# Optimization experiments

Hardware: AMD Instinct MI355X
Metric: run time of the kernel (lower is better)

The kernel has to match this reference:

```python
import jax, jax.numpy as jnp
import numpy as np

N_HEAD = 12
N_EMBD = 768

def setup_inputs() -> dict:
    key = jax.random.key(0)
    ks = jax.random.split(key, 5)
    B, T, C = 4, 2048, N_EMBD
    x = jax.random.normal(ks[0], (B, T, C), dtype=jnp.float32)
    # PyTorch Linear default init ~ U(-1/sqrt(fan_in), 1/sqrt(fan_in)); use small normals for a clean baseline
    s = 1.0 / np.sqrt(C)
    W_attn = jax.random.uniform(ks[1], (C, 3 * C), minval=-s, maxval=s, dtype=jnp.float32)
    b_attn = jax.random.uniform(ks[2], (3 * C,), minval=-s, maxval=s, dtype=jnp.float32)
    W_o = jax.random.uniform(ks[3], (C, C), minval=-s, maxval=s, dtype=jnp.float32)
    b_o = jax.random.uniform(ks[4], (C,), minval=-s, maxval=s, dtype=jnp.float32)
    return {"x": x, "W_attn": W_attn, "b_attn": b_attn, "W_o": W_o, "b_o": b_o}

def reference(x, W_attn, b_attn, W_o, b_o):
    B, T, C = x.shape
    H = N_HEAD
    D = C // H  # head dim
    qkv = x @ W_attn + b_attn                      # [B,T,3C]
    q, k, v = jnp.split(qkv, 3, axis=-1)           # each [B,T,C]
    q = q.reshape(B, T, H, D).transpose(0, 2, 1, 3)  # [B,H,T,D]
    k = k.reshape(B, T, H, D).transpose(0, 2, 1, 3)
    v = v.reshape(B, T, H, D).transpose(0, 2, 1, 3)
    att = jnp.einsum('bhqd,bhkd->bhqk', q, k) / jnp.sqrt(jnp.asarray(D, x.dtype))
    causal = jnp.tril(jnp.ones((T, T), dtype=bool))
    att = jnp.where(causal, att, jnp.asarray(-jnp.inf, att.dtype))
    att = jax.nn.softmax(att, axis=-1)             # dropout=0.0 -> identity
    y = jnp.einsum('bhqk,bhkd->bhqd', att, v)      # [B,H,T,D]
    y = y.transpose(0, 2, 1, 3).reshape(B, T, C)   # [B,T,C]
    return y @ W_o + b_o
```

## Files before the change

### kernel.cpp

```cpp
#include <hip/hip_runtime.h>
#include <hip/hip_bf16.h>

#define NHEAD 12
#define TSEQ 2048
#define CEMB 768
#define DHEAD 64
#define NBATCH 4

typedef __attribute__((ext_vector_type(8))) short bf16x8;
typedef __attribute__((ext_vector_type(4))) float f32x4;

__device__ __forceinline__ ushort f2bf(float f) {
  union { float f; unsigned u; } v; v.f = f;
  unsigned u = v.u;
  u += 0x7FFFu + ((u >> 16) & 1u);
  return (ushort)(u >> 16);
}

__device__ __forceinline__ unsigned cvt_pk_bf16(float lo, float hi) {
  unsigned r;
  asm("v_cvt_pk_bf16_f32 %0, %1, %2" : "=v"(r) : "v"(lo), "v"(hi));
  return r;
}

__device__ __forceinline__ float exp2_raw(float x) {
  float r;
  asm("v_exp_f32 %0, %1" : "=v"(r) : "v"(x));
  return r;
}

__device__ __forceinline__ void lds_fence() {
  asm volatile("s_waitcnt lgkmcnt(0)" ::: "memory");
  __builtin_amdgcn_sched_barrier(0);
}

__global__ __launch_bounds__(256)
void prep(const float* __restrict__ x, ushort* __restrict__ xb,
          const float* __restrict__ Wa, ushort* __restrict__ WaT,
          const float* __restrict__ Wo, ushort* __restrict__ WoT)
{
  __shared__ float tile[32][33];
  const int bid = blockIdx.x, t = threadIdx.x;
  if (bid < 3072) {
    int i = (bid * 256 + t) * 8;
    float4 v0 = *(const float4*)(x + i);
    float4 v1 = *(const float4*)(x + i + 4);
    bf16x8 wv;
    wv[0] = (short)f2bf(v0.x); wv[1] = (short)f2bf(v0.y);
    wv[2] = (short)f2bf(v0.z); wv[3] = (short)f2bf(v0.w);
    wv[4] = (short)f2bf(v1.x); wv[5] = (short)f2bf(v1.y);
    wv[6] = (short)f2bf(v1.z); wv[7] = (short)f2bf(v1.w);
    *(bf16x8*)(xb + i) = wv;
    return;
  }
  const int b2 = bid - 3072;
  const int bx = b2 % 96, by = b2 / 96;
  const int tx = t & 31, ty = t >> 5;
  const float* src; ushort* dst; int C, c0;
  if (bx < 72) { src = Wa; dst = WaT; C = 3 * CEMB; c0 = bx * 32; }
  else         { src = Wo; dst = WoT; C = CEMB;     c0 = (bx - 72) * 32; }
  const int r0 = by * 32;
#pragma unroll
  for (int j = 0; j < 4; ++j)
    tile[ty + j * 8][tx] = src[(size_t)(r0 + ty + j * 8) * C + c0 + tx];
  __syncthreads();
#pragma unroll
  for (int j = 0; j < 4; ++j)
    dst[(size_t)(c0 + ty + j * 8) * CEMB + r0 + tx] = f2bf(tile[tx][ty + j * 8]);
}

__global__ void transpose_v(const ushort* __restrict__ src, ushort* __restrict__ dst) {
  __shared__ ushort tile[32][33];
  int bh = blockIdx.z;
  int t0 = blockIdx.x * 32, d0 = blockIdx.y * 32;
  int tx = threadIdx.x, ty = threadIdx.y;
  const ushort* s = src + (size_t)bh * TSEQ * DHEAD;
  ushort* o = dst + (size_t)bh * TSEQ * DHEAD;
#pragma unroll
  for (int j = 0; j < 4; ++j)
    tile[ty + j * 8][tx] = s[(t0 + ty + j * 8) * DHEAD + d0 + tx];
  __syncthreads();
#pragma unroll
  for (int j = 0; j < 4; ++j)
    o[(size_t)(d0 + ty + j * 8) * TSEQ + t0 + tx] = tile[tx][ty + j * 8];
}

template<int EPI>
__global__ __launch_bounds__(256)
void gemm_bf16(const ushort* __restrict__ A, const ushort* __restrict__ BT,
               const float* __restrict__ bias, float* __restrict__ outF,
               ushort* __restrict__ qd, ushort* __restrict__ kd, ushort* __restrict__ vd,
               int M, int N, int K)
{
  __shared__ __align__(16) char smem[32768];
  const int t = threadIdx.x;
  const int lane = t & 63, wv = t >> 6;
  const int cc = lane & 15, gg = lane >> 4;
  const int m0 = blockIdx.y * 128, n0 = blockIdx.x * 128;
  const int wm = (wv >> 1) * 64, wn = (wv & 1) * 64;

  const int o0 = wv * 1024 + lane * 16;
  const int o1 = o0 + 4096;
  const int r0s = o0 >> 6, s0s = (o0 >> 4) & 3;
  const int r1s = o1 >> 6, s1s = (o1 >> 4) & 3;
  const size_t Kb = (size_t)K * 2;
  const char* a0p = (const char*)A  + (size_t)(m0 + r0s) * Kb + ((s0s ^ ((r0s >> 1) & 3)) << 4);
  const char* a1p = (const char*)A  + (size_t)(m0 + r1s) * Kb + ((s1s ^ ((r1s >> 1) & 3)) << 4);
  const char* b0p = (const char*)BT + (size_t)(n0 + r0s) * Kb + ((s0s ^ ((r0s >> 1) & 3)) << 4);
  const char* b1p = (const char*)BT + (size_t)(n0 + r1s) * Kb + ((s1s ^ ((r1s >> 1) & 3)) << 4);

  auto stage_g = [&](int p, int kb) {
    char* As = smem + p * 16384;
    char* Bs = As + 8192;
    __builtin_amdgcn_global_load_lds(
        (const __attribute__((address_space(1))) unsigned*)(a0p + kb),
        (__attribute__((address_space(3))) unsigned*)(As + wv * 1024), 16, 0, 0);
    __builtin_amdgcn_global_load_lds(
        (const __attribute__((address_space(1))) unsigned*)(a1p + kb),
        (__attribute__((address_space(3))) unsigned*)(As + wv * 1024 + 4096), 16, 0, 0);
    __builtin_amdgcn_global_load_lds(
        (const __attribute__((address_space(1))) unsigned*)(b0p + kb),
        (__attribute__((address_space(3))) unsigned*)(Bs + wv * 1024), 16, 0, 0);
    __builtin_amdgcn_global_load_lds(
        (const __attribute__((address_space(1))) unsigned*)(b1p + kb),
        (__attribute__((address_space(3))) unsigned*)(Bs + wv * 1024 + 4096), 16, 0, 0);
  };

  f32x4 acc[4][4];
#pragma unroll
  for (int i = 0; i < 4; ++i)
#pragma unroll
    for (int j = 0; j < 4; ++j) acc[i][j] = (f32x4){0.f, 0.f, 0.f, 0.f};

  const int KB = K * 2;
  stage_g(0, 0);
  asm volatile("s_waitcnt vmcnt(0)" ::: "memory");
  __syncthreads();
  int p = 0;
  for (int kb = 0; kb < KB; kb += 64) {
    if (kb + 64 < KB) stage_g(p ^ 1, kb + 64);
    const char* As = smem + p * 16384;
    const char* Bs = As + 8192;
    bf16x8 fa[4], fb[4];
#pragma unroll
    for (int i = 0; i < 4; ++i) {
      const int r = wm + i * 16 + cc;
      fa[i] = *(const bf16x8*)(As + r * 64 + ((gg ^ ((r >> 1) & 3)) << 4));
    }
#pragma unroll
    for (int j = 0; j < 4; ++j) {
      const int r = wn + j * 16 + cc;
      fb[j] = *(const bf16x8*)(Bs + r * 64 + ((gg ^ ((r >> 1) & 3)) << 4));
    }
    __builtin_amdgcn_s_setprio(1);
#pragma unroll
    for (int i = 0; i < 4; ++i)
#pragma unroll
      for (int j = 0; j < 4; ++j)
        acc[i][j] = __builtin_amdgcn_mfma_f32_16x16x32_bf16(fa[i], fb[j], acc[i][j], 0, 0, 0);
    __builtin_amdgcn_s_setprio(0);
    asm volatile("s_waitcnt vmcnt(0)" ::: "memory");
    __syncthreads();
    p ^= 1;
  }

#pragma unroll
  for (int i = 0; i < 4; ++i) {
#pragma unroll
    for (int j = 0; j < 4; ++j) {
      int gm0 = m0 + wm + i * 16 + gg * 4;
      int gn  = n0 + wn + j * 16 + cc;
      float bv = bias[gn];
      if (EPI == 0) {
#pragma unroll
        for (int e = 0; e < 4; ++e)
          outF[(size_t)(gm0 + e) * N + gn] = acc[i][j][e] + bv;
      } else {
        int which = gn / CEMB;
        int r = gn - which * CEMB;
        int hh = r >> 6, dd = r & 63;
        ushort* dst = which == 0 ? qd : (which == 1 ? kd : vd);
        float sc = (which == 0) ? 0.125f * 1.4426950408889634f : 1.0f;
#pragma unroll
        for (int e = 0; e < 4; ++e) {
          int gm = gm0 + e;
          int tt = gm & (TSEQ - 1), bb = gm >> 11;
          dst[(size_t)((bb * NHEAD + hh) * TSEQ + tt) * DHEAD + dd] = f2bf((acc[i][j][e] + bv) * sc);
        }
      }
    }
  }
}

__global__ __launch_bounds__(256)
void attn_fwd(const ushort* __restrict__ qg, const ushort* __restrict__ kg,
              const ushort* __restrict__ vTg, ushort* __restrict__ ybb)
{
  __shared__ __align__(16) char smem[40960];
  const int t = threadIdx.x, lane = t & 63, w = t >> 6;
  const int cc = lane & 15, gg = lane >> 4;
  const int NT = TSEQ / 64;
  const int L = blockIdx.x;
  const int r9 = L >> 3;
  const int bx = r9 & 15;
  const int bh = (L & 7) + 8 * (r9 >> 4);
  const int b = bh / NHEAD, h = bh - b * NHEAD;

  const char* Kg = (const char*)(kg + (size_t)bh * TSEQ * DHEAD);
  const char* Vg = (const char*)(vTg + (size_t)bh * TSEQ * DHEAD);

  const int srow = lane >> 3;
  const int ssw  = ((lane & 7) * 16) ^ (srow << 4);

  ushort* Pw = (ushort*)(smem + 32768 + w * 2048);
  const int sw8 = (cc & 7) << 3;

  auto stage = [&](int pp, int kt) {
#pragma unroll
    for (int i = 0; i < 2; ++i) {
      const int c = w * 2 + i;
      const char* gk = Kg + (size_t)(kt * 64 + c * 8 + srow) * 128 + ssw;
      __builtin_amdgcn_global_load_lds(
          (const __attribute__((address_space(1))) unsigned*)gk,
          (__attribute__((address_space(3))) unsigned*)(smem + pp * 8192 + c * 1024),
          16, 0, 0);
      const char* gv = Vg + (size_t)(c * 8 + srow) * (TSEQ * 2) + (size_t)kt * 128 + ssw;
      __builtin_amdgcn_global_load_lds(
          (const __attribute__((address_space(1))) unsigned*)gv,
          (__attribute__((address_space(3))) unsigned*)(smem + 16384 + pp * 8192 + c * 1024),
          16, 0, 0);
    }
  };

  int p = 0;
  for (int pass = 0; pass < 2; ++pass) {
    const int qt = pass ? (NT - 1 - bx) : bx;
    const int qrow0 = qt * 64 + w * 16;

    const ushort* Qp = qg + ((size_t)bh * TSEQ + qrow0) * DHEAD;
    bf16x8 fq0 = *(const bf16x8*)(Qp + cc * DHEAD + 8 * gg);
    bf16x8 fq1 = *(const bf16x8*)(Qp + cc * DHEAD + 32 + 8 * gg);

    f32x4 o[4];
#pragma unroll
    for (int i = 0; i < 4; ++i) o[i] = (f32x4){0.f, 0.f, 0.f, 0.f};
    float m = -1e30f, l = 0.f;

    stage(p, 0);
    asm volatile("s_waitcnt vmcnt(0)" ::: "memory");
    __syncthreads();

    for (int kt = 0; kt <= qt; ++kt) {
      if (kt < qt) stage(p ^ 1, kt + 1);

      const char* Kl = smem + p * 8192;
      const char* Vl = smem + 16384 + p * 8192;
      f32x4 st[4];
#pragma unroll
      for (int ct = 0; ct < 4; ++ct) st[ct] = (f32x4){0.f, 0.f, 0.f, 0.f};
      __builtin_amdgcn_s_setprio(1);
#pragma unroll
      for (int ct = 0; ct < 4; ++ct) {
        const int r = ct * 16 + cc;
        const char* kb = Kl + r * 128;
        bf16x8 fk0 = *(const bf16x8*)(kb + ((gg * 16) ^ ((r & 7) << 4)));
        bf16x8 fk1 = *(const bf16x8*)(kb + ((64 + gg * 16) ^ ((r & 7) << 4)));
        st[ct] = __builtin_amdgcn_mfma_f32_16x16x32_bf16(fk0, fq0, st[ct], 0, 0, 0);
        st[ct] = __builtin_amdgcn_mfma_f32_16x16x32_bf16(fk1, fq1, st[ct], 0, 0, 0);
      }
      __builtin_amdgcn_s_setprio(0);

      if (kt == qt) {
#pragma unroll
        for (int ct = 0; ct < 4; ++ct)
#pragma unroll
          for (int e = 0; e < 4; ++e)
            if (ct * 16 + gg * 4 + e > w * 16 + cc) st[ct][e] = -1e30f;
      }
      float ml = st[0][0];
#pragma unroll
      for (int ct = 0; ct < 4; ++ct)
#pragma unroll
        for (int e = 0; e < 4; ++e) ml = fmaxf(ml, st[ct][e]);
      ml = fmaxf(ml, __shfl_xor(ml, 16, 64));
      ml = fmaxf(ml, __shfl_xor(ml, 32, 64));
      float mn = m;
      if (!__all(ml - m <= 11.54f)) {
        mn = fmaxf(m, ml);
        float al = exp2_raw(m - mn);
#pragma unroll
        for (int dt = 0; dt < 4; ++dt)
#pragma unroll
          for (int e = 0; e < 4; ++e) o[dt][e] *= al;
        l *= al;
        m = mn;
      }
      float ps = 0.f;
#pragma unroll
      for (int ct = 0; ct < 4; ++ct)
#pragma unroll
        for (int e = 0; e < 4; ++e) { float pp = exp2_raw(st[ct][e] - mn); st[ct][e] = pp; ps += pp; }
#pragma unroll
      for (int ct = 0; ct < 4; ++ct) {
        uint2 pw;
        pw.x = cvt_pk_bf16(st[ct][0], st[ct][1]);
        pw.y = cvt_pk_bf16(st[ct][2], st[ct][3]);
        *(uint2*)&Pw[cc * 64 + ((ct * 16 + gg * 4) ^ sw8)] = pw;
      }
      ps += __shfl_xor(ps, 16, 64);
      ps += __shfl_xor(ps, 32, 64);
      l += ps;
      lds_fence();
      __builtin_amdgcn_s_setprio(1);
#pragma unroll
      for (int kc = 0; kc < 2; ++kc) {
        bf16x8 pb = *(const bf16x8*)&Pw[cc * 64 + ((kc * 32 + 8 * gg) ^ sw8)];
#pragma unroll
        for (int dt = 0; dt < 4; ++dt) {
          const int rd = dt * 16 + cc;
          bf16x8 fv = *(const bf16x8*)(Vl + rd * 128 + ((kc * 64 + gg * 16) ^ ((rd & 7) << 4)));
          o[dt] = __builtin_amdgcn_mfma_f32_16x16x32_bf16(fv, pb, o[dt], 0, 0, 0);
        }
      }
      __builtin_amdgcn_s_setprio(0);
      asm volatile("s_waitcnt vmcnt(0)" ::: "memory");
      __syncthreads();
      p ^= 1;
    }

    float inv = 1.0f / l;
    ushort* yrow = ybb + (size_t)(b * TSEQ + qrow0 + cc) * CEMB + h * DHEAD;
#pragma unroll
    for (int dt = 0; dt < 4; ++dt) {
      uint2 pw;
      pw.x = cvt_pk_bf16(o[dt][0] * inv, o[dt][1] * inv);
      pw.y = cvt_pk_bf16(o[dt][2] * inv, o[dt][3] * inv);
      *(uint2*)(yrow + dt * 16 + gg * 4) = pw;
    }
  }
}

extern "C" void kernel_launch(void* const* d_in, const int* in_sizes, int n_in,
                              void* d_out, int out_size, void* d_ws, size_t ws_size,
                              hipStream_t stream)
{
  (void)in_sizes; (void)n_in; (void)out_size; (void)ws_size;
  const float* x  = (const float*)d_in[0];
  const float* Wa = (const float*)d_in[1];
  const float* ba = (const float*)d_in[2];
  const float* Wo = (const float*)d_in[3];
  const float* bo = (const float*)d_in[4];
  float* out = (float*)d_out;

  char* p = (char*)d_ws;
  ushort* WaT  = (ushort*)p; p += (size_t)3 * CEMB * CEMB * 2;
  ushort* WoT  = (ushort*)p; p += (size_t)CEMB * CEMB * 2;
  ushort* xb   = (ushort*)p; p += (size_t)NBATCH * TSEQ * CEMB * 2;
  ushort* qb   = (ushort*)p; p += (size_t)NBATCH * NHEAD * TSEQ * DHEAD * 2;
  ushort* kb   = (ushort*)p; p += (size_t)NBATCH * NHEAD * TSEQ * DHEAD * 2;
  ushort* vtmp = (ushort*)p; p += (size_t)NBATCH * NHEAD * TSEQ * DHEAD * 2;
  ushort* vT   = (ushort*)p; p += (size_t)NBATCH * NHEAD * TSEQ * DHEAD * 2;
  ushort* yb   = (ushort*)p; p += (size_t)NBATCH * TSEQ * CEMB * 2;

  prep<<<3072 + 96 * 24, 256, 0, stream>>>(x, xb, Wa, WaT, Wo, WoT);
  gemm_bf16<1><<<dim3(3 * CEMB / 128, NBATCH * TSEQ / 128), 256, 0, stream>>>(
      xb, WaT, ba, nullptr, qb, kb, vtmp, NBATCH * TSEQ, 3 * CEMB, CEMB);
  transpose_v<<<dim3(TSEQ / 32, DHEAD / 32, NBATCH * NHEAD), dim3(32, 8), 0, stream>>>(vtmp, vT);
  attn_fwd<<<dim3(TSEQ / 128 * NBATCH * NHEAD), 256, 0, stream>>>(qb, kb, vT, yb);
  gemm_bf16<0><<<dim3(CEMB / 128, NBATCH * TSEQ / 128), 256, 0, stream>>>(
      yb, WoT, bo, out, nullptr, nullptr, nullptr, NBATCH * TSEQ, CEMB, CEMB);
}
```

Baseline: 133.7 us.

## Fuse V transpose into QKV epilogue and software-pipeline PV MFMA in attention

The QKV GEMM epilogue now writes V directly in transposed [bh][d][t] layout with packed 4-element stores, so the separate transpose_v kernel launch and its temporary buffer go away. In attention, K and V staging are split, and the P·V MFMA for the previous key tile is deferred into the next iteration after the QK^T MFMAs. P is double-buffered per wave to make this possible. The aim is to overlap softmax latency with matrix work and to drop the LDS fence. The cost is more LDS (48KB), which may reduce occupancy, and an extra epilogue PV step after the loop.

```diff
diff --git a/kernel.cpp b/kernel.cpp
--- a/kernel.cpp
+++ b/kernel.cpp
@@ -27,11 +27,6 @@
   float r;
   asm("v_exp_f32 %0, %1" : "=v"(r) : "v"(x));
   return r;
-}
-
-__device__ __forceinline__ void lds_fence() {
-  asm volatile("s_waitcnt lgkmcnt(0)" ::: "memory");
-  __builtin_amdgcn_sched_barrier(0);
 }
 
 __global__ __launch_bounds__(256)
@@ -69,22 +64,6 @@
     dst[(size_t)(c0 + ty + j * 8) * CEMB + r0 + tx] = f2bf(tile[tx][ty + j * 8]);
 }
 
-__global__ void transpose_v(const ushort* __restrict__ src, ushort* __restrict__ dst) {
-  __shared__ ushort tile[32][33];
-  int bh = blockIdx.z;
-  int t0 = blockIdx.x * 32, d0 = blockIdx.y * 32;
-  int tx = threadIdx.x, ty = threadIdx.y;
-  const ushort* s = src + (size_t)bh * TSEQ * DHEAD;
-  ushort* o = dst + (size_t)bh * TSEQ * DHEAD;
-#pragma unroll
-  for (int j = 0; j < 4; ++j)
-    tile[ty + j * 8][tx] = s[(t0 + ty + j * 8) * DHEAD + d0 + tx];
-  __syncthreads();
-#pragma unroll
-  for (int j = 0; j < 4; ++j)
-    o[(size_t)(d0 + ty + j * 8) * TSEQ + t0 + tx] = tile[tx][ty + j * 8];
-}
-
 template<int EPI>
 __global__ __launch_bounds__(256)
 void gemm_bf16(const ushort* __restrict__ A, const ushort* __restrict__ BT,
@@ -179,13 +158,20 @@
         int which = gn / CEMB;
         int r = gn - which * CEMB;
         int hh = r >> 6, dd = r & 63;
-        ushort* dst = which == 0 ? qd : (which == 1 ? kd : vd);
-        float sc = (which == 0) ? 0.125f * 1.4426950408889634f : 1.0f;
-#pragma unroll
-        for (int e = 0; e < 4; ++e) {
-          int gm = gm0 + e;
-          int tt = gm & (TSEQ - 1), bb = gm >> 11;
-          dst[(size_t)((bb * NHEAD + hh) * TSEQ + tt) * DHEAD + dd] = f2bf((acc[i][j][e] + bv) * sc);
+        int tt0 = gm0 & (TSEQ - 1), bb = gm0 >> 11;
+        if (which == 2) {
+          ushort* dstv = vd + ((size_t)((bb * NHEAD + hh) * DHEAD + dd)) * TSEQ + tt0;
+          uint2 pw;
+          pw.x = cvt_pk_bf16(acc[i][j][0] + bv, acc[i][j][1] + bv);
+          pw.y = cvt_pk_bf16(acc[i][j][2] + bv, acc[i][j][3] + bv);
+          *(uint2*)dstv = pw;
+        } else {
+          ushort* dst = which == 0 ? qd : kd;
+          float sc = (which == 0) ? 0.125f * 1.4426950408889634f : 1.0f;
+#pragma unroll
+          for (int e = 0; e < 4; ++e)
+            dst[(size_t)((bb * NHEAD + hh) * TSEQ + tt0 + e) * DHEAD + dd] =
+                f2bf((acc[i][j][e] + bv) * sc);
         }
       }
     }
@@ -196,7 +182,7 @@
 void attn_fwd(const ushort* __restrict__ qg, const ushort* __restrict__ kg,
               const ushort* __restrict__ vTg, ushort* __restrict__ ybb)
 {
-  __shared__ __align__(16) char smem[40960];
+  __shared__ __align__(16) char smem[49152];
   const int t = threadIdx.x, lane = t & 63, w = t >> 6;
   const int cc = lane & 15, gg = lane >> 4;
   const int NT = TSEQ / 64;
@@ -212,22 +198,28 @@
   const int srow = lane >> 3;
   const int ssw  = ((lane & 7) * 16) ^ (srow << 4);
 
-  ushort* Pw = (ushort*)(smem + 32768 + w * 2048);
+  ushort* Pw = (ushort*)(smem + 32768 + w * 4096);
   const int sw8 = (cc & 7) << 3;
 
-  auto stage = [&](int pp, int kt) {
+  auto stageK = [&](int pb, int kt) {
 #pragma unroll
     for (int i = 0; i < 2; ++i) {
       const int c = w * 2 + i;
       const char* gk = Kg + (size_t)(kt * 64 + c * 8 + srow) * 128 + ssw;
       __builtin_amdgcn_global_load_lds(
           (const __attribute__((address_space(1))) unsigned*)gk,
-          (__attribute__((address_space(3))) unsigned*)(smem + pp * 8192 + c * 1024),
+          (__attribute__((address_space(3))) unsigned*)(smem + pb * 8192 + c * 1024),
           16, 0, 0);
+    }
+  };
+  auto stageV = [&](int pb, int kt) {
+#pragma unroll
+    for (int i = 0; i < 2; ++i) {
+      const int c = w * 2 + i;
       const char* gv = Vg + (size_t)(c * 8 + srow) * (TSEQ * 2) + (size_t)kt * 128 + ssw;
       __builtin_amdgcn_global_load_lds(
           (const __attribute__((address_space(1))) unsigned*)gv,
-          (__attribute__((address_space(3))) unsigned*)(smem + 16384 + pp * 8192 + c * 1024),
+          (__attribute__((address_space(3))) unsigned*)(smem + 16384 + pb * 8192 + c * 1024),
           16, 0, 0);
     }
   };
@@ -246,15 +238,15 @@
     for (int i = 0; i < 4; ++i) o[i] = (f32x4){0.f, 0.f, 0.f, 0.f};
     float m = -1e30f, l = 0.f;
 
-    stage(p, 0);
+    stageK(p, 0);
     asm volatile("s_waitcnt vmcnt(0)" ::: "memory");
     __syncthreads();
 
     for (int kt = 0; kt <= qt; ++kt) {
-      if (kt < qt) stage(p ^ 1, kt + 1);
+      if (kt < qt) stageK(p ^ 1, kt + 1);
+      stageV(p, kt);
 
       const char* Kl = smem + p * 8192;
-      const char* Vl = smem + 16384 + p * 8192;
       f32x4 st[4];
 #pragma unroll
       for (int ct = 0; ct < 4; ++ct) st[ct] = (f32x4){0.f, 0.f, 0.f, 0.f};
@@ -268,6 +260,21 @@
         st[ct] = __builtin_amdgcn_mfma_f32_16x16x32_bf16(fk0, fq0, st[ct], 0, 0, 0);
         st[ct] = __builtin_amdgcn_mfma_f32_16x16x32_bf16(fk1, fq1, st[ct], 0, 0, 0);
       }
+
+      if (kt > 0) {
+        const char* Vprev = smem + 16384 + (p ^ 1) * 8192;
+        const ushort* Pprev = Pw + (p ^ 1) * 1024;
+#pragma unroll
+        for (int kc = 0; kc < 2; ++kc) {
+          bf16x8 pb = *(const bf16x8*)&Pprev[cc * 64 + ((kc * 32 + 8 * gg) ^ sw8)];
+#pragma unroll
+          for (int dt = 0; dt < 4; ++dt) {
+            const int rd = dt * 16 + cc;
+            bf16x8 fv = *(const bf16x8*)(Vprev + rd * 128 + ((kc * 64 + gg * 16) ^ ((rd & 7) << 4)));
+            o[dt] = __builtin_amdgcn_mfma_f32_16x16x32_bf16(fv, pb, o[dt], 0, 0, 0);
+          }
+        }
+      }
       __builtin_amdgcn_s_setprio(0);
 
       if (kt == qt) {
@@ -305,27 +312,30 @@
         uint2 pw;
         pw.x = cvt_pk_bf16(st[ct][0], st[ct][1]);
         pw.y = cvt_pk_bf16(st[ct][2], st[ct][3]);
-        *(uint2*)&Pw[cc * 64 + ((ct * 16 + gg * 4) ^ sw8)] = pw;
+        *(uint2*)&Pw[p * 1024 + cc * 64 + ((ct * 16 + gg * 4) ^ sw8)] = pw;
       }
       ps += __shfl_xor(ps, 16, 64);
       ps += __shfl_xor(ps, 32, 64);
       l += ps;
-      lds_fence();
-      __builtin_amdgcn_s_setprio(1);
-#pragma unroll
-      for (int kc = 0; kc < 2; ++kc) {
-        bf16x8 pb = *(const bf16x8*)&Pw[cc * 64 + ((kc * 32 + 8 * gg) ^ sw8)];
-#pragma unroll
-        for (int dt = 0; dt < 4; ++dt) {
-          const int rd = dt * 16 + cc;
-          bf16x8 fv = *(const bf16x8*)(Vl + rd * 128 + ((kc * 64 + gg * 16) ^ ((rd & 7) << 4)));
-          o[dt] = __builtin_amdgcn_mfma_f32_16x16x32_bf16(fv, pb, o[dt], 0, 0, 0);
-        }
-      }
-      __builtin_amdgcn_s_setprio(0);
+
       asm volatile("s_waitcnt vmcnt(0)" ::: "memory");
       __syncthreads();
       p ^= 1;
+    }
+
+    {
+      const char* Vlast = smem + 16384 + (p ^ 1) * 8192;
+      const ushort* Plast = Pw + (p ^ 1) * 1024;
+#pragma unroll
+      for (int kc = 0; kc < 2; ++kc) {
+        bf16x8 pb = *(const bf16x8*)&Plast[cc * 64 + ((kc * 32 + 8 * gg) ^ sw8)];
+#pragma unroll
+        for (int dt = 0; dt < 4; ++dt) {
+          const int rd = dt * 16 + cc;
+          bf16x8 fv = *(const bf16x8*)(Vlast + rd * 128 + ((kc * 64 + gg * 16) ^ ((rd & 7) << 4)));
+          o[dt] = __builtin_amdgcn_mfma_f32_16x16x32_bf16(fv, pb, o[dt], 0, 0, 0);
+        }
+      }
     }
 
     float inv = 1.0f / l;
@@ -358,14 +368,12 @@
   ushort* xb   = (ushort*)p; p += (size_t)NBATCH * TSEQ * CEMB * 2;
   ushort* qb   = (ushort*)p; p += (size_t)NBATCH * NHEAD * TSEQ * DHEAD * 2;
   ushort* kb   = (ushort*)p; p += (size_t)NBATCH * NHEAD * TSEQ * DHEAD * 2;
-  ushort* vtmp = (ushort*)p; p += (size_t)NBATCH * NHEAD * TSEQ * DHEAD * 2;
   ushort* vT   = (ushort*)p; p += (size_t)NBATCH * NHEAD * TSEQ * DHEAD * 2;
   ushort* yb   = (ushort*)p; p += (size_t)NBATCH * TSEQ * CEMB * 2;
 
   prep<<<3072 + 96 * 24, 256, 0, stream>>>(x, xb, Wa, WaT, Wo, WoT);
   gemm_bf16<1><<<dim3(3 * CEMB / 128, NBATCH * TSEQ / 128), 256, 0, stream>>>(
-      xb, WaT, ba, nullptr, qb, kb, vtmp, NBATCH * TSEQ, 3 * CEMB, CEMB);
-  transpose_v<<<dim3(TSEQ / 32, DHEAD / 32, NBATCH * NHEAD), dim3(32, 8), 0, stream>>>(vtmp, vT);
+      xb, WaT, ba, nullptr, qb, kb, vT, NBATCH * TSEQ, 3 * CEMB, CEMB);
   attn_fwd<<<dim3(TSEQ / 128 * NBATCH * NHEAD), 256, 0, stream>>>(qb, kb, vT, yb);
   gemm_bf16<0><<<dim3(CEMB / 128, NBATCH * TSEQ / 128), 256, 0, stream>>>(
       yb, WoT, bo, out, nullptr, nullptr, nullptr, NBATCH * TSEQ, CEMB, CEMB);
```

New measurement: 132.7 us. No clear change (-0.7%).
